# Kernel tuning notes

Hardware: AMD Instinct MI355X
Metric: run time of the kernel (lower is better)

## Reference

```python
import jax, jax.numpy as jnp
import numpy as np

USER_NUM = 100000
ITEM_NUM = 50000
N_NODES = USER_NUM + ITEM_NUM
NNZ = 1200000
BATCH = 4096
HIDDEN = 64
N_LAYERS = 4
ALPHA = [0.25, 0.25, 0.25, 0.25]


def setup_inputs() -> dict:
    key = jax.random.key(0)
    k1, k2, k3, k4, k5, k6, k7 = jax.random.split(key, 7)
    user = jax.random.randint(k1, (BATCH,), 0, USER_NUM, dtype=jnp.int64 if jax.config.jax_enable_x64 else jnp.int32)
    item = jax.random.randint(k2, (BATCH,), 0, ITEM_NUM, dtype=user.dtype)
    src = jax.random.randint(k3, (NNZ,), 0, N_NODES, dtype=user.dtype)
    dst = jax.random.randint(k4, (NNZ,), 0, N_NODES, dtype=user.dtype)
    edge_w = jax.random.uniform(k5, (NNZ,), dtype=jnp.float32)
    user_emb = jax.random.normal(k6, (USER_NUM, HIDDEN), dtype=jnp.float32)
    item_emb = jax.random.normal(k7, (ITEM_NUM, HIDDEN), dtype=jnp.float32)
    return {"user": user, "item": item, "src": src, "dst": dst,
            "edge_w": edge_w, "user_emb": user_emb, "item_emb": item_emb}


def _spmm(src, dst, edge_w, x):
    # y[dst] += w * x[src]  (COO SpMM over fixed normalized adjacency)
    return jax.ops.segment_sum(edge_w[:, None] * x[src], dst, num_segments=N_NODES)


def reference(user, item, src, dst, edge_w, user_emb, item_emb):
    emb = jnp.concatenate([user_emb, item_emb], axis=0)          # [N, d]
    sum_emb = ALPHA[0] * emb
    cur = emb
    for layer in range(1, N_LAYERS):
        cur = _spmm(src, dst, edge_w, cur)
        sum_emb = sum_emb + ALPHA[layer] * cur
    all_user = sum_emb[:USER_NUM]
    all_item = sum_emb[USER_NUM:]
    gamma = jnp.sum(all_user[user] * all_item[item], axis=1)     # [B]
    return jax.nn.sigmoid(gamma)
```

## Files before the change

kernel.cpp:

```cpp
#include <hip/hip_runtime.h>
#include <hip/hip_fp16.h>

#define USER_NUM 100000
#define ITEM_NUM 50000
#define N_NODES  150000
#define NNZ      1200000
#define BATCH    4096
#define HIDDEN   64

#define BUCK_SHIFT 10
#define NBUCK 147
#define BCAP  10240
#define BINA_CHUNK 4096
#define NBINA ((NNZ + BINA_CHUNK - 1) / BINA_CHUNK)
#define TOTAL8 (N_NODES * HIDDEN / 8)
#define CONVB ((TOTAL8 + 255) / 256)

__device__ __forceinline__ unsigned pack2(float a, float b) {
    __half2 h = __floats2half2_rn(a, b);
    return *(unsigned*)&h;
}
__device__ __forceinline__ float4 unpack4(uint2 u) {
    __half2 h0 = *(__half2*)&u.x;
    __half2 h1 = *(__half2*)&u.y;
    float2 f0 = __half22float2(h0);
    float2 f1 = __half22float2(h1);
    return make_float4(f0.x, f0.y, f1.x, f1.y);
}

__global__ void init_kernel(int* __restrict__ cursorB) {
    if (threadIdx.x < NBUCK) cursorB[threadIdx.x] = 0;
}

__global__ void convbinA_kernel(const int* __restrict__ src, const int* __restrict__ dst,
                                const float* __restrict__ ew,
                                int* __restrict__ cursorB, int2* __restrict__ binned,
                                const float* __restrict__ ue, const float* __restrict__ ie,
                                uint4* __restrict__ embh) {
    if (blockIdx.x >= NBINA) {
        int idx = (blockIdx.x - NBINA) * blockDim.x + threadIdx.x;
        if (idx >= TOTAL8) return;
        const int usz8 = USER_NUM * HIDDEN / 8;
        const float4* base = (idx < usz8) ? (const float4*)ue + (size_t)idx * 2
                                          : (const float4*)ie + (size_t)(idx - usz8) * 2;
        float4 a = base[0], b = base[1];
        embh[idx] = make_uint4(pack2(a.x, a.y), pack2(a.z, a.w),
                               pack2(b.x, b.y), pack2(b.z, b.w));
        return;
    }
    __shared__ int hist[NBUCK];
    __shared__ int base[NBUCK];
    const int chunk0 = blockIdx.x * BINA_CHUNK;
    for (int i = threadIdx.x; i < NBUCK; i += 256) hist[i] = 0;
    __syncthreads();
    for (int k = 0; k < BINA_CHUNK / 256; ++k) {
        int e = chunk0 + k * 256 + threadIdx.x;
        if (e < NNZ) atomicAdd(&hist[dst[e] >> BUCK_SHIFT], 1);
    }
    __syncthreads();
    for (int i = threadIdx.x; i < NBUCK; i += 256) {
        int c = hist[i];
        base[i] = c ? atomicAdd(&cursorB[i], c) : 0;
        hist[i] = 0;
    }
    __syncthreads();
    for (int k = 0; k < BINA_CHUNK / 256; ++k) {
        int e = chunk0 + k * 256 + threadIdx.x;
        if (e < NNZ) {
            int d = dst[e];
            int b = d >> BUCK_SHIFT;
            int r = atomicAdd(&hist[b], 1);
            binned[(size_t)b * BCAP + base[b] + r] =
                make_int2(src[e] | ((d & 1023) << 18), __float_as_int(ew[e]));
        }
    }
}

__global__ __launch_bounds__(1024) void binB_kernel(const int2* __restrict__ binned,
                                                    const int* __restrict__ cursorB,
                                                    int* __restrict__ rowp,
                                                    int2* __restrict__ srcw) {
    __shared__ int hist[1 << BUCK_SHIFT];
    __shared__ int sb[256];
    __shared__ int wsum[16];
    const int b = blockIdx.x;
    const int tid = threadIdx.x;
    hist[tid] = 0;
    if (tid < 256) sb[tid] = (tid < NBUCK) ? cursorB[tid] : 0;
    __syncthreads();
    for (int off = 1; off < 256; off <<= 1) {
        int t2 = 0;
        if (tid < 256 && tid >= off) t2 = sb[tid - off];
        __syncthreads();
        if (tid < 256) sb[tid] += t2;
        __syncthreads();
    }
    const int bucketBase = (b == 0) ? 0 : sb[b - 1];
    const int cnt = cursorB[b];
    const size_t lo = (size_t)b * BCAP;
    for (int i = tid; i < cnt; i += 1024)
        atomicAdd(&hist[(unsigned)binned[lo + i].x >> 18], 1);
    __syncthreads();
    const int v = hist[tid];
    const int lane = tid & 63, w = tid >> 6;
    int x = v;
    for (int off = 1; off < 64; off <<= 1) {
        int y = __shfl_up(x, off, 64);
        if (lane >= off) x += y;
    }
    if (lane == 63) wsum[w] = x;
    __syncthreads();
    if (tid < 16) {
        int orig = wsum[tid];
        int s = orig;
        for (int off = 1; off < 16; off <<= 1) {
            int y = __shfl_up(s, off, 64);
            if (tid >= off) s += y;
        }
        wsum[tid] = s - orig;
    }
    __syncthreads();
    const int excl = bucketBase + (x - v) + wsum[w];
    const int nodeBase = b << BUCK_SHIFT;
    if (nodeBase + tid < N_NODES) rowp[nodeBase + tid] = excl;
    if (b == 0 && tid == 0) rowp[N_NODES] = NNZ;
    hist[tid] = excl;
    __syncthreads();
    for (int i = tid; i < cnt; i += 1024) {
        int2 p = binned[lo + i];
        int dl = (unsigned)p.x >> 18;
        int pos = atomicAdd(&hist[dl], 1);
        srcw[pos] = make_int2(p.x & 0x3FFFF, p.y);
    }
}

__device__ __forceinline__ float4 gather_node_v4(int start, int end, int gl,
                                                 const int2* __restrict__ srcw,
                                                 const uint2* __restrict__ rows) {
    float4 acc = make_float4(0.f, 0.f, 0.f, 0.f);
    for (int base = start; base < end; base += 16) {
        int2 e = make_int2(0, 0);
        if (base + gl < end) e = srcw[base + gl];
        int m = end - base; if (m > 16) m = 16;
        for (int j0 = 0; j0 < m; j0 += 8) {
            const uint2* bp[8];
            float w[8];
            #pragma unroll
            for (int k = 0; k < 8; ++k) {
                int idx = j0 + k;
                int ss = __shfl(e.x, idx, 16);
                float ww = __int_as_float(__shfl(e.y, idx, 16));
                bool valid = idx < m;
                ss = valid ? ss : 0;
                w[k] = valid ? ww : 0.f;
                bp[k] = rows + (size_t)ss * 16 + gl;
            }
            uint2 v[8];
            #pragma unroll
            for (int k = 0; k < 8; ++k) v[k] = *bp[k];
            #pragma unroll
            for (int k = 0; k < 8; ++k) {
                float4 f = unpack4(v[k]);
                acc.x = fmaf(w[k], f.x, acc.x);
                acc.y = fmaf(w[k], f.y, acc.y);
                acc.z = fmaf(w[k], f.z, acc.z);
                acc.w = fmaf(w[k], f.w, acc.w);
            }
        }
    }
    return acc;
}

__global__ void spmm_gather_kernel(const int* __restrict__ rowp,
                                   const int2* __restrict__ srcw,
                                   const uint2* __restrict__ embh,
                                   uint2* __restrict__ c1h) {
    int wid = (blockIdx.x * blockDim.x + threadIdx.x) >> 6;
    int lane = threadIdx.x & 63;
    int grp = lane >> 4, gl = lane & 15;
    int n = wid * 4 + grp;
    bool act = (n < N_NODES);
    int start = 0, end = 0;
    if (act) { start = rowp[n]; end = rowp[n + 1]; }
    float4 acc = gather_node_v4(start, end, gl, srcw, embh);
    if (act) c1h[(size_t)n * 16 + gl] = make_uint2(pack2(acc.x, acc.y), pack2(acc.z, acc.w));
}

__global__ void twohop_kernel(const int* __restrict__ user, const int* __restrict__ item,
                              const int* __restrict__ rowp, const int2* __restrict__ srcw,
                              const uint2* __restrict__ c1h,
                              const float* __restrict__ user_emb,
                              const float* __restrict__ item_emb,
                              float* __restrict__ sums) {
    int wid = (blockIdx.x * blockDim.x + threadIdx.x) >> 6;
    int lane = threadIdx.x & 63;
    int grp = lane >> 4, gl = lane & 15;
    if (wid >= 2 * BATCH) return;
    int t = wid;
    int n = (t < BATCH) ? user[t] : USER_NUM + item[t - BATCH];
    int s1 = rowp[n], e1 = rowp[n + 1];
    float4 acc = make_float4(0.f, 0.f, 0.f, 0.f);
    for (int jb = s1 + grp; jb < e1; jb += 4) {
        int2 ej = srcw[jb];
        int sj = ej.x;
        float wj = __int_as_float(ej.y);
        float4 f1 = unpack4(c1h[(size_t)sj * 16 + gl]);
        float4 inner = gather_node_v4(rowp[sj], rowp[sj + 1], gl, srcw, c1h);
        acc.x = fmaf(wj, f1.x + inner.x, acc.x);
        acc.y = fmaf(wj, f1.y + inner.y, acc.y);
        acc.z = fmaf(wj, f1.z + inner.z, acc.z);
        acc.w = fmaf(wj, f1.w + inner.w, acc.w);
    }
    for (int m = 16; m < 64; m <<= 1) {
        acc.x += __shfl_xor(acc.x, m, 64);
        acc.y += __shfl_xor(acc.y, m, 64);
        acc.z += __shfl_xor(acc.z, m, 64);
        acc.w += __shfl_xor(acc.w, m, 64);
    }
    if (grp == 0) {
        const float* ebase = (n < USER_NUM) ? user_emb + (size_t)n * HIDDEN
                                            : item_emb + (size_t)(n - USER_NUM) * HIDDEN;
        float4 ev = *(const float4*)(ebase + gl * 4);
        float4 cv = unpack4(c1h[(size_t)n * 16 + gl]);
        float4 o = make_float4(ev.x + cv.x + acc.x, ev.y + cv.y + acc.y,
                               ev.z + cv.z + acc.z, ev.w + cv.w + acc.w);
        *(float4*)(sums + (size_t)t * HIDDEN + gl * 4) = o;
    }
}

__global__ void dot_kernel(const float* __restrict__ sums, float* __restrict__ out) {
    int b = blockIdx.x * (blockDim.x >> 6) + (threadIdx.x >> 6);
    int lane = threadIdx.x & 63;
    if (b >= BATCH) return;
    float su = sums[(size_t)b * HIDDEN + lane];
    float si = sums[(size_t)(BATCH + b) * HIDDEN + lane];
    float p = su * si;
    for (int off = 32; off > 0; off >>= 1) p += __shfl_down(p, off, 64);
    if (lane == 0) {
        float g = 0.0625f * p;
        out[b] = 1.0f / (1.0f + expf(-g));
    }
}

extern "C" void kernel_launch(void* const* d_in, const int* in_sizes, int n_in,
                              void* d_out, int out_size, void* d_ws, size_t ws_size,
                              hipStream_t stream) {
    const int*   user     = (const int*)d_in[0];
    const int*   item     = (const int*)d_in[1];
    const int*   src      = (const int*)d_in[2];
    const int*   dst      = (const int*)d_in[3];
    const float* ew       = (const float*)d_in[4];
    const float* user_emb = (const float*)d_in[5];
    const float* item_emb = (const float*)d_in[6];
    float* out = (float*)d_out;

    float* sums    = (float*)d_ws;
    uint2* embh    = (uint2*)(sums + (size_t)2 * BATCH * HIDDEN);
    uint2* c1h     = embh + (size_t)N_NODES * 16;
    int2*  srcw    = (int2*)(c1h + (size_t)N_NODES * 16);
    int2*  binned  = srcw + NNZ + 16;
    int*   rowp    = (int*)(binned + (size_t)NBUCK * BCAP);
    int*   cursorB = rowp + N_NODES + 1;

    init_kernel<<<1, 256, 0, stream>>>(cursorB);

    convbinA_kernel<<<NBINA + CONVB, 256, 0, stream>>>(
        src, dst, ew, cursorB, binned, user_emb, item_emb, (uint4*)embh);

    binB_kernel<<<NBUCK, 1024, 0, stream>>>(binned, cursorB, rowp, srcw);

    const int nodesPerBlock = 16;
    const int nGatherBlocks = (N_NODES + nodesPerBlock - 1) / nodesPerBlock;
    spmm_gather_kernel<<<nGatherBlocks, 256, 0, stream>>>(rowp, srcw, embh, c1h);

    twohop_kernel<<<(2 * BATCH * 64) / 256, 256, 0, stream>>>(
        user, item, rowp, srcw, c1h, user_emb, item_emb, sums);

    dot_kernel<<<(BATCH * 64 + 255) / 256, 256, 0, stream>>>(sums, out);
}
```

Measured before the change: 103.8 us.

## Replace global atomic bucket cursors with count, scan, place binning passes

The single binning kernel, which reserved bucket slots through global atomicAdd on shared cursors, is split into a per-chunk histogram kernel, a per-bucket exclusive scan across chunks, and a placement kernel. This removes the global atomic contention and the init kernel, and makes the binned order deterministic. In exchange it adds two kernel launches and a second read of dst.

```diff
diff --git a/kernel.cpp b/kernel.cpp
--- a/kernel.cpp
+++ b/kernel.cpp
@@ -28,15 +28,10 @@
     return make_float4(f0.x, f0.y, f1.x, f1.y);
 }
 
-__global__ void init_kernel(int* __restrict__ cursorB) {
-    if (threadIdx.x < NBUCK) cursorB[threadIdx.x] = 0;
-}
-
-__global__ void convbinA_kernel(const int* __restrict__ src, const int* __restrict__ dst,
-                                const float* __restrict__ ew,
-                                int* __restrict__ cursorB, int2* __restrict__ binned,
-                                const float* __restrict__ ue, const float* __restrict__ ie,
-                                uint4* __restrict__ embh) {
+__global__ void convcount_kernel(const int* __restrict__ dst,
+                                 int* __restrict__ H,
+                                 const float* __restrict__ ue, const float* __restrict__ ie,
+                                 uint4* __restrict__ embh) {
     if (blockIdx.x >= NBINA) {
         int idx = (blockIdx.x - NBINA) * blockDim.x + threadIdx.x;
         if (idx >= TOTAL8) return;
@@ -49,7 +44,6 @@
         return;
     }
     __shared__ int hist[NBUCK];
-    __shared__ int base[NBUCK];
     const int chunk0 = blockIdx.x * BINA_CHUNK;
     for (int i = threadIdx.x; i < NBUCK; i += 256) hist[i] = 0;
     __syncthreads();
@@ -58,10 +52,44 @@
         if (e < NNZ) atomicAdd(&hist[dst[e] >> BUCK_SHIFT], 1);
     }
     __syncthreads();
+    for (int i = threadIdx.x; i < NBUCK; i += 256) H[blockIdx.x * NBUCK + i] = hist[i];
+}
+
+__global__ void bin_scan_kernel(int* __restrict__ H, int* __restrict__ cursorB) {
+    __shared__ int lds[256];
+    __shared__ int carry;
+    const int b = blockIdx.x;
+    if (threadIdx.x == 0) carry = 0;
+    __syncthreads();
+    for (int t0 = 0; t0 < NBINA; t0 += 256) {
+        int j = t0 + threadIdx.x;
+        int v = (j < NBINA) ? H[j * NBUCK + b] : 0;
+        lds[threadIdx.x] = v;
+        __syncthreads();
+        for (int off = 1; off < 256; off <<= 1) {
+            int t = (threadIdx.x >= off) ? lds[threadIdx.x - off] : 0;
+            __syncthreads();
+            lds[threadIdx.x] += t;
+            __syncthreads();
+        }
+        int excl = lds[threadIdx.x] - v + carry;
+        if (j < NBINA) H[j * NBUCK + b] = excl;
+        __syncthreads();
+        if (threadIdx.x == 255) carry += lds[255];
+        __syncthreads();
+    }
+    if (threadIdx.x == 0) cursorB[b] = carry;
+}
+
+__global__ void place_kernel(const int* __restrict__ src, const int* __restrict__ dst,
+                             const float* __restrict__ ew,
+                             const int* __restrict__ H, int2* __restrict__ binned) {
+    __shared__ int rank[NBUCK];
+    __shared__ int base[NBUCK];
+    const int chunk0 = blockIdx.x * BINA_CHUNK;
     for (int i = threadIdx.x; i < NBUCK; i += 256) {
-        int c = hist[i];
-        base[i] = c ? atomicAdd(&cursorB[i], c) : 0;
-        hist[i] = 0;
+        base[i] = H[blockIdx.x * NBUCK + i];
+        rank[i] = 0;
     }
     __syncthreads();
     for (int k = 0; k < BINA_CHUNK / 256; ++k) {
@@ -69,7 +97,7 @@
         if (e < NNZ) {
             int d = dst[e];
             int b = d >> BUCK_SHIFT;
-            int r = atomicAdd(&hist[b], 1);
+            int r = atomicAdd(&rank[b], 1);
             binned[(size_t)b * BCAP + base[b] + r] =
                 make_int2(src[e] | ((d & 1023) << 18), __float_as_int(ew[e]));
         }
@@ -261,11 +289,14 @@
     int2*  binned  = srcw + NNZ + 16;
     int*   rowp    = (int*)(binned + (size_t)NBUCK * BCAP);
     int*   cursorB = rowp + N_NODES + 1;
-
-    init_kernel<<<1, 256, 0, stream>>>(cursorB);
-
-    convbinA_kernel<<<NBINA + CONVB, 256, 0, stream>>>(
-        src, dst, ew, cursorB, binned, user_emb, item_emb, (uint4*)embh);
+    int*   H       = cursorB + NBUCK;
+
+    convcount_kernel<<<NBINA + CONVB, 256, 0, stream>>>(
+        dst, H, user_emb, item_emb, (uint4*)embh);
+
+    bin_scan_kernel<<<NBUCK, 256, 0, stream>>>(H, cursorB);
+
+    place_kernel<<<NBINA, 256, 0, stream>>>(src, dst, ew, H, binned);
 
     binB_kernel<<<NBUCK, 1024, 0, stream>>>(binned, cursorB, rowp, srcw);
 
```

Result: no change. 102.5 us (-1.2%).
